# Kernel optimization log

Measured on AMD Instinct MI355X. Metric: run time of the kernel, lower is better.

The kernel has to match this reference:

```python
import jax, jax.numpy as jnp
import numpy as np

B, N, D, K = 16, 512, 64, 8  # batch, num_nodes, node_dim, num_edge_class


def setup_inputs() -> dict:
    key = jax.random.key(0)
    ks = jax.random.split(key, 6)
    return {
        "node_states": jax.random.normal(ks[0], (B, N, D), jnp.float32),
        "adjacency_in": jax.random.randint(ks[1], (B, N, N), 0, K + 1, jnp.int32),
        "distance": jax.random.normal(ks[2], (B, N, N), jnp.float32),  # declared but unused, as in source
        "matrices_in": jax.random.normal(ks[3], (K, D, D), jnp.float32) * 0.1,
        "matrices_out": jax.random.normal(ks[4], (K, D, D), jnp.float32) * 0.1,
        "message_bias": jax.random.normal(ks[5], (2 * D,), jnp.float32) * 0.1,
    }


def reference(node_states, adjacency_in, distance, matrices_in, matrices_out, message_bias):
    # node_states: [B, N, D]; adjacency_in: [B, N, N] int in [0, K]; 0 = no edge.
    node_dim = node_states.shape[-1]
    zeros = jnp.zeros((1, node_dim, node_dim), node_states.dtype)
    Min = jnp.concatenate([zeros, matrices_in], axis=0)    # [K+1, D, D]
    Mout = jnp.concatenate([zeros, matrices_out], axis=0)  # [K+1, D, D]
    # Transform every node state by every edge-type matrix once:
    # T[b, j, k, d] = sum_e M[k, d, e] * h[b, j, e]
    T_in = jnp.einsum('kde,bje->bjkd', Min, node_states)
    T_out = jnp.einsum('kde,bje->bjkd', Mout, node_states)
    # One-hot edge types: oh[b, i, j, k] = [adjacency_in[b, i, j] == k]
    oh = jax.nn.one_hot(adjacency_in, Min.shape[0], dtype=node_states.dtype)  # [B, N, N, K+1]
    # a_in_mul[b, i, d]  = sum_j M_in[adj[b,i,j]]  @ h[b, j]  (identical math to the
    # dense [B, N*D, N*D] block-matmul in the TF source, without materializing it)
    a_in_mul = jnp.einsum('bijk,bjkd->bid', oh, T_in)
    # a_out uses the transposed adjacency: adj_out[b,i,j] = adj[b,j,i]
    a_out_mul = jnp.einsum('bjik,bjkd->bid', oh, T_out)
    messages = jnp.concatenate([a_in_mul, a_out_mul], axis=-1) + message_bias
    return messages  # [B, N, 2*D]
```

## Files before the change

### kernel.cpp

```cpp
#include <hip/hip_runtime.h>

#define B_ 16
#define N_ 512
#define D_ 64
#define K_ 8

#define WSU_BYTES ((size_t)B_ * N_ * N_ * 2)
#define T_BYTES   ((size_t)B_ * N_ * (K_ + 1) * D_ * 2)
#define HBF_BYTES ((size_t)B_ * N_ * D_ * 2)
#define MBF_BYTES ((size_t)2 * K_ * D_ * D_ * 2)
#define TROWB 1152

typedef __attribute__((ext_vector_type(8))) short bf8_t;
typedef __attribute__((ext_vector_type(4))) float f4_t;

__device__ __forceinline__ unsigned short f2bf(float x) {
  union { float f; unsigned u; } c; c.f = x;
  unsigned r = c.u + 0x7FFFu + ((c.u >> 16) & 1u);
  return (unsigned short)(r >> 16);
}

__global__ __launch_bounds__(256) void conv_inputs(
    const float* __restrict__ h, const float* __restrict__ Min,
    const float* __restrict__ Mout,
    unsigned short* __restrict__ hbf, unsigned short* __restrict__ Mbf,
    unsigned short* __restrict__ Tin, unsigned short* __restrict__ Tout) {
  const int g = blockIdx.x * 256 + threadIdx.x;
  {
    const float4 v = ((const float4*)h)[g];
    ushort4 o; o.x = f2bf(v.x); o.y = f2bf(v.y); o.z = f2bf(v.z); o.w = f2bf(v.w);
    ((ushort4*)hbf)[g] = o;
  }
  if (g < 8192) {
    const float4 v = ((const float4*)Min)[g];
    ushort4 o; o.x = f2bf(v.x); o.y = f2bf(v.y); o.z = f2bf(v.z); o.w = f2bf(v.w);
    ((ushort4*)Mbf)[g] = o;
  } else if (g < 16384) {
    const int t = g - 8192;
    const float4 v = ((const float4*)Mout)[t];
    ushort4 o; o.x = f2bf(v.x); o.y = f2bf(v.y); o.z = f2bf(v.z); o.w = f2bf(v.w);
    ((ushort4*)Mbf)[8192 + t] = o;
  }
  {
    const int row = g >> 4, part = g & 15;
    const ushort4 z = make_ushort4(0, 0, 0, 0);
    ((ushort4*)(Tin  + (size_t)row * 576))[part] = z;
    ((ushort4*)(Tout + (size_t)row * 576))[part] = z;
  }
}

__global__ __launch_bounds__(256) void prep_adj(const int* __restrict__ adj,
                                                unsigned short* __restrict__ wsu) {
  __shared__ int ta[64][65];
  __shared__ int tb[64][65];
  const int blk = blockIdx.x;
  const int xcd = blk & 7, rest = blk >> 3;
  const int b = xcd + 8 * (rest & 1);
  const int tile = rest >> 1;
  const int i0 = (tile >> 3) * 64, j0 = (tile & 7) * 64;
  const int lane = threadIdx.x & 63, w = threadIdx.x >> 6;
  const int* ab = adj + (size_t)b * N_ * N_;
#pragma unroll
  for (int r = w; r < 64; r += 4) {
    ta[r][lane] = ab[(size_t)(i0 + r) * N_ + j0 + lane];
    tb[r][lane] = ab[(size_t)(j0 + r) * N_ + i0 + lane];
  }
  __syncthreads();
  unsigned short* wb = wsu + (size_t)b * N_ * N_;
#pragma unroll
  for (int r = w; r < 64; r += 4) {
    wb[(size_t)(i0 + r) * N_ + j0 + lane] =
        (unsigned short)(ta[r][lane] | (tb[lane][r] << 8));
  }
}

__global__ __launch_bounds__(256) void build_T_mfma(
    const unsigned short* __restrict__ hbf,
    const unsigned short* __restrict__ Mbf,
    unsigned short* __restrict__ Tin,
    unsigned short* __restrict__ Tout) {
  const int blk = blockIdx.x;
  const int b   = (blk & 7) + 8 * ((blk >> 3) & 1);
  const int u   = blk >> 4;
  const int jt  = u & 15;
  const int kdt = u >> 4;
  const int w = threadIdx.x >> 6, l = threadIdx.x & 63;
  const int j0  = jt * 32;
  const int kd0 = kdt * 256 + w * 64;
  const int r16 = l & 15, grp = l >> 4;

  const unsigned short* ha = hbf + ((size_t)b * N_ + j0 + r16) * 64 + grp * 8;
  bf8_t afr[2][2];
#pragma unroll
  for (int fr = 0; fr < 2; ++fr)
#pragma unroll
    for (int ks = 0; ks < 2; ++ks)
      afr[fr][ks] = *(const bf8_t*)(ha + fr * 16 * 64 + ks * 32);

  const unsigned short* mb = Mbf + (size_t)(kd0 + r16) * 64 + grp * 8;
  bf8_t bfr[4][2];
#pragma unroll
  for (int fc = 0; fc < 4; ++fc)
#pragma unroll
    for (int ks = 0; ks < 2; ++ks)
      bfr[fc][ks] = *(const bf8_t*)(mb + fc * 16 * 64 + ks * 32);

  f4_t acc[2][4];
#pragma unroll
  for (int fr = 0; fr < 2; ++fr)
#pragma unroll
    for (int fc = 0; fc < 4; ++fc) acc[fr][fc] = (f4_t)(0.f);

#pragma unroll
  for (int fr = 0; fr < 2; ++fr)
#pragma unroll
    for (int fc = 0; fc < 4; ++fc) {
      acc[fr][fc] = __builtin_amdgcn_mfma_f32_16x16x32_bf16(
          afr[fr][0], bfr[fc][0], acc[fr][fc], 0, 0, 0);
      acc[fr][fc] = __builtin_amdgcn_mfma_f32_16x16x32_bf16(
          afr[fr][1], bfr[fc][1], acc[fr][fc], 0, 0, 0);
    }

  unsigned short* Tbase = (kd0 >= 512) ? Tout : Tin;
  const int kdl0 = kd0 & 511;
  unsigned short* trow = Tbase + (size_t)b * N_ * 576 + 64;
#pragma unroll
  for (int fr = 0; fr < 2; ++fr)
#pragma unroll
    for (int fc = 0; fc < 4; ++fc) {
      const int kd = kdl0 + fc * 16 + r16;
#pragma unroll
      for (int r = 0; r < 4; ++r) {
        const int j = j0 + fr * 16 + grp * 4 + r;
        trow[(size_t)j * 576 + kd] = f2bf(acc[fr][fc][r]);
      }
    }
}

__global__ __launch_bounds__(512) void gather_msg(
    const unsigned short* __restrict__ wsu,
    const unsigned short* __restrict__ Tin,
    const unsigned short* __restrict__ Tout,
    const float* __restrict__ bias,
    float* __restrict__ out) {
  __shared__ int4 ed4[1024];
  const int blk = blockIdx.x;
  const int b  = (blk & 7) + 8 * ((blk >> 3) & 1);
  const int i0 = (blk >> 4) * 16;
  const int tid = threadIdx.x;
  const int w = tid >> 6, lane = tid & 63;
  const int half = lane >> 5, lane5 = lane & 31;

  const int4* src = (const int4*)(wsu + ((size_t)b * N_ + i0) * N_);
  ed4[tid]       = src[tid];
  ed4[tid + 512] = src[tid + 512];
  __syncthreads();

  const unsigned short* edrow =
      (const unsigned short*)ed4 + (2 * w + half) * N_;

  const char* tinb  = (const char*)Tin  + (size_t)b * N_ * TROWB;
  const char* toutb = (const char*)Tout + (size_t)b * N_ * TROWB;
  unsigned voff = (unsigned)lane5 * 4;
  float aI0 = 0.f, aI1 = 0.f, aO0 = 0.f, aO1 = 0.f;
#pragma unroll 8
  for (int j = 0; j < N_; ++j) {
    const unsigned v = edrow[j];
    const unsigned ui = *(const unsigned*)(tinb  + (voff + ((v & 0xFFu) << 7)));
    const unsigned uo = *(const unsigned*)(toutb + (voff + ((v >> 8) << 7)));
    aI0 += __uint_as_float(ui << 16);
    aI1 += __uint_as_float(ui & 0xFFFF0000u);
    aO0 += __uint_as_float(uo << 16);
    aO1 += __uint_as_float(uo & 0xFFFF0000u);
    voff += TROWB;
  }

  const int row = i0 + 2 * w + half;
  const int d = lane5 * 2;
  float* orow = out + ((size_t)b * N_ + row) * (2 * D_);
  const float2 bi = *(const float2*)(bias + d);
  const float2 bo = *(const float2*)(bias + D_ + d);
  *(float2*)(orow + d)      = make_float2(aI0 + bi.x, aI1 + bi.y);
  *(float2*)(orow + D_ + d) = make_float2(aO0 + bo.x, aO1 + bo.y);
}

#define ACCUM(kv, bucket) switch (kv) { \
    case 1: (bucket)[0] += v_; break; case 2: (bucket)[1] += v_; break; \
    case 3: (bucket)[2] += v_; break; case 4: (bucket)[3] += v_; break; \
    case 5: (bucket)[4] += v_; break; case 6: (bucket)[5] += v_; break; \
    case 7: (bucket)[6] += v_; break; case 8: (bucket)[7] += v_; break; \
    default: break; }

__global__ __launch_bounds__(64) void ggnn_fallback(
    const float* __restrict__ h, const int* __restrict__ adj,
    const float* __restrict__ Min, const float* __restrict__ Mout,
    const float* __restrict__ bias, float* __restrict__ out) {
  const int blk = blockIdx.x;
  const int b  = blk / (N_ / 2);
  const int i0 = (blk % (N_ / 2)) * 2;
  const int d  = threadIdx.x;
  float s_in[2][K_], s_out[2][K_];
#pragma unroll
  for (int r = 0; r < 2; ++r)
#pragma unroll
    for (int k = 0; k < K_; ++k) { s_in[r][k] = 0.f; s_out[r][k] = 0.f; }
  const int* rowp0 = adj + (b * N_ + i0) * N_;
  const int* rowp1 = rowp0 + N_;
  const int* colp  = adj + b * N_ * N_ + i0;
  const float* hb  = h + b * N_ * D_ + d;
  for (int j0 = 0; j0 < N_; j0 += 8) {
    float hv[8]; int kr0[8], kr1[8], kc0[8], kc1[8];
#pragma unroll
    for (int m = 0; m < 8; ++m) {
      hv[m] = hb[(j0 + m) * D_];
      kr0[m] = rowp0[j0 + m]; kr1[m] = rowp1[j0 + m];
      kc0[m] = colp[(j0 + m) * N_]; kc1[m] = colp[(j0 + m) * N_ + 1];
    }
#pragma unroll
    for (int m = 0; m < 8; ++m) {
      const float v_ = hv[m];
      ACCUM(kr0[m], s_in[0]); ACCUM(kr1[m], s_in[1]);
      ACCUM(kc0[m], s_out[0]); ACCUM(kc1[m], s_out[1]);
    }
  }
  __shared__ float S[2][2][K_][D_];
#pragma unroll
  for (int r = 0; r < 2; ++r)
#pragma unroll
    for (int k = 0; k < K_; ++k) { S[r][0][k][d] = s_in[r][k]; S[r][1][k][d] = s_out[r][k]; }
  __syncthreads();
  float acc_in[2], acc_out[2];
#pragma unroll
  for (int r = 0; r < 2; ++r) { acc_in[r] = bias[d]; acc_out[r] = bias[D_ + d]; }
  for (int k = 0; k < K_; ++k) {
#pragma unroll
    for (int e0 = 0; e0 < D_; e0 += 4) {
      const float4 mi = *(const float4*)(Min  + (k * D_ + d) * D_ + e0);
      const float4 mo = *(const float4*)(Mout + (k * D_ + d) * D_ + e0);
#pragma unroll
      for (int r = 0; r < 2; ++r) {
        const float4 si = *(const float4*)(&S[r][0][k][e0]);
        const float4 so = *(const float4*)(&S[r][1][k][e0]);
        acc_in[r]  += mi.x * si.x + mi.y * si.y + mi.z * si.z + mi.w * si.w;
        acc_out[r] += mo.x * so.x + mo.y * so.y + mo.z * so.z + mo.w * so.w;
      }
    }
  }
#pragma unroll
  for (int r = 0; r < 2; ++r) {
    out[(b * N_ + i0 + r) * (2 * D_) + d]      = acc_in[r];
    out[(b * N_ + i0 + r) * (2 * D_) + D_ + d] = acc_out[r];
  }
}

extern "C" void kernel_launch(void* const* d_in, const int* in_sizes, int n_in,
                              void* d_out, int out_size, void* d_ws, size_t ws_size,
                              hipStream_t stream) {
  const float* h    = (const float*)d_in[0];
  const int*   adj  = (const int*)d_in[1];
  const float* Min  = (const float*)d_in[3];
  const float* Mout = (const float*)d_in[4];
  const float* bias = (const float*)d_in[5];
  float* out = (float*)d_out;

  if (ws_size < WSU_BYTES + 2 * T_BYTES + HBF_BYTES + MBF_BYTES) {
    hipLaunchKernelGGL(ggnn_fallback, dim3(B_ * N_ / 2), dim3(64), 0, stream,
                       h, adj, Min, Mout, bias, out);
    return;
  }
  unsigned short* wsu  = (unsigned short*)d_ws;
  unsigned short* Tin  = (unsigned short*)((char*)d_ws + WSU_BYTES);
  unsigned short* Tout = (unsigned short*)((char*)d_ws + WSU_BYTES + T_BYTES);
  unsigned short* hbf  = (unsigned short*)((char*)d_ws + WSU_BYTES + 2 * T_BYTES);
  unsigned short* Mbf  = (unsigned short*)((char*)d_ws + WSU_BYTES + 2 * T_BYTES + HBF_BYTES);

  hipLaunchKernelGGL(conv_inputs,  dim3(512),  dim3(256), 0, stream,
                     h, Min, Mout, hbf, Mbf, Tin, Tout);
  hipLaunchKernelGGL(prep_adj,     dim3(1024), dim3(256), 0, stream, adj, wsu);
  hipLaunchKernelGGL(build_T_mfma, dim3(1024), dim3(256), 0, stream, hbf, Mbf, Tin, Tout);
  hipLaunchKernelGGL(gather_msg,   dim3(512),  dim3(512), 0, stream,
                     wsu, Tin, Tout, bias, out);
}
```

Before: 158.4 us.

## Split gather over j-halves with atomics, widen per-lane loads, precompute byte offsets

The gather kernel now splits the neighbour loop into two halves across blocks. Each lane handles 8 feature columns with 16-byte loads, and partial sums go into a zeroed output through atomicAdd. The adjacency workspace is widened to 32-bit entries that hold precomputed byte offsets for the in and out tables, which removes shift/mask arithmetic from the inner loop. build_T is retiled so each wave computes a 16x64 tile with packed 8-byte stores. The aim is more memory-level parallelism and fewer gather instructions, at the cost of a doubled adjacency workspace, extra output zeroing and atomic traffic.

```diff
diff --git a/kernel.cpp b/kernel.cpp
--- a/kernel.cpp
+++ b/kernel.cpp
@@ -5,7 +5,7 @@
 #define D_ 64
 #define K_ 8
 
-#define WSU_BYTES ((size_t)B_ * N_ * N_ * 2)
+#define WSU_BYTES ((size_t)B_ * N_ * N_ * 4)
 #define T_BYTES   ((size_t)B_ * N_ * (K_ + 1) * D_ * 2)
 #define HBF_BYTES ((size_t)B_ * N_ * D_ * 2)
 #define MBF_BYTES ((size_t)2 * K_ * D_ * D_ * 2)
@@ -24,7 +24,8 @@
     const float* __restrict__ h, const float* __restrict__ Min,
     const float* __restrict__ Mout,
     unsigned short* __restrict__ hbf, unsigned short* __restrict__ Mbf,
-    unsigned short* __restrict__ Tin, unsigned short* __restrict__ Tout) {
+    unsigned short* __restrict__ Tin, unsigned short* __restrict__ Tout,
+    float* __restrict__ out) {
   const int g = blockIdx.x * 256 + threadIdx.x;
   {
     const float4 v = ((const float4*)h)[g];
@@ -47,10 +48,15 @@
     ((ushort4*)(Tin  + (size_t)row * 576))[part] = z;
     ((ushort4*)(Tout + (size_t)row * 576))[part] = z;
   }
+  {
+    const float4 z4 = make_float4(0.f, 0.f, 0.f, 0.f);
+    ((float4*)out)[g]          = z4;
+    ((float4*)out)[g + 131072] = z4;
+  }
 }
 
 __global__ __launch_bounds__(256) void prep_adj(const int* __restrict__ adj,
-                                                unsigned short* __restrict__ wsu) {
+                                                unsigned* __restrict__ wsu) {
   __shared__ int ta[64][65];
   __shared__ int tb[64][65];
   const int blk = blockIdx.x;
@@ -66,11 +72,11 @@
     tb[r][lane] = ab[(size_t)(j0 + r) * N_ + i0 + lane];
   }
   __syncthreads();
-  unsigned short* wb = wsu + (size_t)b * N_ * N_;
+  unsigned* wb = wsu + (size_t)b * N_ * N_;
 #pragma unroll
   for (int r = w; r < 64; r += 4) {
     wb[(size_t)(i0 + r) * N_ + j0 + lane] =
-        (unsigned short)(ta[r][lane] | (tb[lane][r] << 8));
+        (unsigned)(ta[r][lane] << 7) | ((unsigned)tb[lane][r] << 23);
   }
 }
 
@@ -82,106 +88,116 @@
   const int blk = blockIdx.x;
   const int b   = (blk & 7) + 8 * ((blk >> 3) & 1);
   const int u   = blk >> 4;
-  const int jt  = u & 15;
-  const int kdt = u >> 4;
+  const int kdt = u >> 3;
+  const int jt4 = u & 7;
   const int w = threadIdx.x >> 6, l = threadIdx.x & 63;
-  const int j0  = jt * 32;
-  const int kd0 = kdt * 256 + w * 64;
+  const int j0  = (jt4 * 4 + w) * 16;
+  const int kd0 = kdt * 64;
   const int r16 = l & 15, grp = l >> 4;
 
-  const unsigned short* ha = hbf + ((size_t)b * N_ + j0 + r16) * 64 + grp * 8;
-  bf8_t afr[2][2];
-#pragma unroll
-  for (int fr = 0; fr < 2; ++fr)
-#pragma unroll
-    for (int ks = 0; ks < 2; ++ks)
-      afr[fr][ks] = *(const bf8_t*)(ha + fr * 16 * 64 + ks * 32);
-
-  const unsigned short* mb = Mbf + (size_t)(kd0 + r16) * 64 + grp * 8;
-  bf8_t bfr[4][2];
-#pragma unroll
-  for (int fc = 0; fc < 4; ++fc)
-#pragma unroll
-    for (int ks = 0; ks < 2; ++ks)
-      bfr[fc][ks] = *(const bf8_t*)(mb + fc * 16 * 64 + ks * 32);
-
-  f4_t acc[2][4];
-#pragma unroll
-  for (int fr = 0; fr < 2; ++fr)
-#pragma unroll
-    for (int fc = 0; fc < 4; ++fc) acc[fr][fc] = (f4_t)(0.f);
-
-#pragma unroll
-  for (int fr = 0; fr < 2; ++fr)
-#pragma unroll
-    for (int fc = 0; fc < 4; ++fc) {
-      acc[fr][fc] = __builtin_amdgcn_mfma_f32_16x16x32_bf16(
-          afr[fr][0], bfr[fc][0], acc[fr][fc], 0, 0, 0);
-      acc[fr][fc] = __builtin_amdgcn_mfma_f32_16x16x32_bf16(
-          afr[fr][1], bfr[fc][1], acc[fr][fc], 0, 0, 0);
-    }
-
-  unsigned short* Tbase = (kd0 >= 512) ? Tout : Tin;
-  const int kdl0 = kd0 & 511;
-  unsigned short* trow = Tbase + (size_t)b * N_ * 576 + 64;
-#pragma unroll
-  for (int fr = 0; fr < 2; ++fr)
-#pragma unroll
-    for (int fc = 0; fc < 4; ++fc) {
-      const int kd = kdl0 + fc * 16 + r16;
-#pragma unroll
-      for (int r = 0; r < 4; ++r) {
-        const int j = j0 + fr * 16 + grp * 4 + r;
-        trow[(size_t)j * 576 + kd] = f2bf(acc[fr][fc][r]);
-      }
-    }
-}
-
-__global__ __launch_bounds__(512) void gather_msg(
-    const unsigned short* __restrict__ wsu,
+  const unsigned short* hr = hbf + ((size_t)(b * N_ + j0 + r16)) * 64 + grp * 8;
+  bf8_t hfr[2];
+  hfr[0] = *(const bf8_t*)(hr);
+  hfr[1] = *(const bf8_t*)(hr + 32);
+
+  const unsigned short* mr = Mbf + (size_t)(kd0 + r16) * 64 + grp * 8;
+
+  f4_t acc[4];
+#pragma unroll
+  for (int fc = 0; fc < 4; ++fc) acc[fc] = (f4_t)(0.f);
+#pragma unroll
+  for (int fc = 0; fc < 4; ++fc) {
+    const bf8_t a0 = *(const bf8_t*)(mr + (size_t)fc * 16 * 64);
+    const bf8_t a1 = *(const bf8_t*)(mr + (size_t)fc * 16 * 64 + 32);
+    acc[fc] = __builtin_amdgcn_mfma_f32_16x16x32_bf16(a0, hfr[0], acc[fc], 0, 0, 0);
+    acc[fc] = __builtin_amdgcn_mfma_f32_16x16x32_bf16(a1, hfr[1], acc[fc], 0, 0, 0);
+  }
+
+  unsigned short* Tb = ((kd0 & 512) ? Tout : Tin) + (size_t)b * N_ * 576;
+  const int kdl = kd0 & 511;
+  const int j = j0 + r16;
+  unsigned short* trow = Tb + (size_t)j * 576 + 64 + kdl + grp * 4;
+#pragma unroll
+  for (int fc = 0; fc < 4; ++fc) {
+    const unsigned lo = (unsigned)f2bf(acc[fc][0]) | ((unsigned)f2bf(acc[fc][1]) << 16);
+    const unsigned hi = (unsigned)f2bf(acc[fc][2]) | ((unsigned)f2bf(acc[fc][3]) << 16);
+    *(uint2*)(trow + fc * 16) = make_uint2(lo, hi);
+  }
+}
+
+__global__ __launch_bounds__(256) void gather_msg(
+    const unsigned* __restrict__ wsu,
     const unsigned short* __restrict__ Tin,
     const unsigned short* __restrict__ Tout,
     const float* __restrict__ bias,
     float* __restrict__ out) {
-  __shared__ int4 ed4[1024];
+  __shared__ unsigned ed[32][260];
   const int blk = blockIdx.x;
   const int b  = (blk & 7) + 8 * ((blk >> 3) & 1);
-  const int i0 = (blk >> 4) * 16;
+  const int rest = blk >> 4;
+  const int rb = rest & 15;
+  const int jh = rest >> 4;
   const int tid = threadIdx.x;
   const int w = tid >> 6, lane = tid & 63;
-  const int half = lane >> 5, lane5 = lane & 31;
-
-  const int4* src = (const int4*)(wsu + ((size_t)b * N_ + i0) * N_);
-  ed4[tid]       = src[tid];
-  ed4[tid + 512] = src[tid + 512];
+
+  const unsigned* wrow = wsu + ((size_t)(b * N_ + rb * 32)) * N_ + jh * 256;
+#pragma unroll
+  for (int c = 0; c < 8; ++c) {
+    const int idx = c * 256 + tid;
+    const int row = idx >> 6, col4 = idx & 63;
+    *(int4*)&ed[row][col4 * 4] = *(const int4*)(wrow + (size_t)row * N_ + col4 * 4);
+  }
   __syncthreads();
 
-  const unsigned short* edrow =
-      (const unsigned short*)ed4 + (2 * w + half) * N_;
-
-  const char* tinb  = (const char*)Tin  + (size_t)b * N_ * TROWB;
-  const char* toutb = (const char*)Tout + (size_t)b * N_ * TROWB;
-  unsigned voff = (unsigned)lane5 * 4;
-  float aI0 = 0.f, aI1 = 0.f, aO0 = 0.f, aO1 = 0.f;
+  const int row_l = w * 8 + (lane >> 3);
+  const int d0 = (lane & 7) * 8;
+  const unsigned* edrow = &ed[row_l][0];
+  const char* tinB  = (const char*)Tin  + (size_t)b * N_ * TROWB;
+  const char* toutB = (const char*)Tout + (size_t)b * N_ * TROWB;
+  unsigned vbase = (unsigned)(jh * 256) * TROWB + (unsigned)d0 * 2;
+
+  float aI[8], aO[8];
+#pragma unroll
+  for (int q = 0; q < 8; ++q) { aI[q] = 0.f; aO[q] = 0.f; }
+
 #pragma unroll 8
-  for (int j = 0; j < N_; ++j) {
-    const unsigned v = edrow[j];
-    const unsigned ui = *(const unsigned*)(tinb  + (voff + ((v & 0xFFu) << 7)));
-    const unsigned uo = *(const unsigned*)(toutb + (voff + ((v >> 8) << 7)));
-    aI0 += __uint_as_float(ui << 16);
-    aI1 += __uint_as_float(ui & 0xFFFF0000u);
-    aO0 += __uint_as_float(uo << 16);
-    aO1 += __uint_as_float(uo & 0xFFFF0000u);
-    voff += TROWB;
-  }
-
-  const int row = i0 + 2 * w + half;
-  const int d = lane5 * 2;
+  for (int j = 0; j < 256; ++j) {
+    const unsigned wv = edrow[j];
+    const uint4 ti = *(const uint4*)(tinB  + (vbase + (wv & 0xFFFFu)));
+    const uint4 to = *(const uint4*)(toutB + (vbase + (wv >> 16)));
+    aI[0] += __uint_as_float(ti.x << 16);
+    aI[1] += __uint_as_float(ti.x & 0xFFFF0000u);
+    aI[2] += __uint_as_float(ti.y << 16);
+    aI[3] += __uint_as_float(ti.y & 0xFFFF0000u);
+    aI[4] += __uint_as_float(ti.z << 16);
+    aI[5] += __uint_as_float(ti.z & 0xFFFF0000u);
+    aI[6] += __uint_as_float(ti.w << 16);
+    aI[7] += __uint_as_float(ti.w & 0xFFFF0000u);
+    aO[0] += __uint_as_float(to.x << 16);
+    aO[1] += __uint_as_float(to.x & 0xFFFF0000u);
+    aO[2] += __uint_as_float(to.y << 16);
+    aO[3] += __uint_as_float(to.y & 0xFFFF0000u);
+    aO[4] += __uint_as_float(to.z << 16);
+    aO[5] += __uint_as_float(to.z & 0xFFFF0000u);
+    aO[6] += __uint_as_float(to.w << 16);
+    aO[7] += __uint_as_float(to.w & 0xFFFF0000u);
+    vbase += TROWB;
+  }
+
+  if (jh == 0) {
+#pragma unroll
+    for (int q = 0; q < 8; ++q) {
+      aI[q] += bias[d0 + q];
+      aO[q] += bias[D_ + d0 + q];
+    }
+  }
+  const int row = rb * 32 + row_l;
   float* orow = out + ((size_t)b * N_ + row) * (2 * D_);
-  const float2 bi = *(const float2*)(bias + d);
-  const float2 bo = *(const float2*)(bias + D_ + d);
-  *(float2*)(orow + d)      = make_float2(aI0 + bi.x, aI1 + bi.y);
-  *(float2*)(orow + D_ + d) = make_float2(aO0 + bo.x, aO1 + bo.y);
+#pragma unroll
+  for (int q = 0; q < 8; ++q) {
+    atomicAdd(orow + d0 + q, aI[q]);
+    atomicAdd(orow + D_ + d0 + q, aO[q]);
+  }
 }
 
 #define ACCUM(kv, bucket) switch (kv) { \
@@ -268,16 +284,16 @@
                        h, adj, Min, Mout, bias, out);
     return;
   }
-  unsigned short* wsu  = (unsigned short*)d_ws;
+  unsigned*       wsu  = (unsigned*)d_ws;
   unsigned short* Tin  = (unsigned short*)((char*)d_ws + WSU_BYTES);
   unsigned short* Tout = (unsigned short*)((char*)d_ws + WSU_BYTES + T_BYTES);
   unsigned short* hbf  = (unsigned short*)((char*)d_ws + WSU_BYTES + 2 * T_BYTES);
   unsigned short* Mbf  = (unsigned short*)((char*)d_ws + WSU_BYTES + 2 * T_BYTES + HBF_BYTES);
 
   hipLaunchKernelGGL(conv_inputs,  dim3(512),  dim3(256), 0, stream,
-                     h, Min, Mout, hbf, Mbf, Tin, Tout);
+                     h, Min, Mout, hbf, Mbf, Tin, Tout, out);
   hipLaunchKernelGGL(prep_adj,     dim3(1024), dim3(256), 0, stream, adj, wsu);
-  hipLaunchKernelGGL(build_T_mfma, dim3(1024), dim3(256), 0, stream, hbf, Mbf, Tin, Tout);
-  hipLaunchKernelGGL(gather_msg,   dim3(512),  dim3(512), 0, stream,
+  hipLaunchKernelGGL(build_T_mfma, dim3(2048), dim3(256), 0, stream, hbf, Mbf, Tin, Tout);
+  hipLaunchKernelGGL(gather_msg,   dim3(512),  dim3(256), 0, stream,
                      wsu, Tin, Tout, bias, out);
 }
```

After: 234.3 us. +47.9%, slower.
